# Kernel tuning notes

Measured on AMD Instinct MI355X. Metric: run time of the kernel, lower is better.

The kernel has to match this reference:

```python
import jax, jax.numpy as jnp
import numpy as np

B = 128   # batch (must equal input_size due to the transpose quirk in the source)
S = 1024  # sequence length
D = 128   # input_size
H = 256   # hidden_size


def setup_inputs() -> dict:
    key = jax.random.key(0)
    k_x, k_wf, k_wb = jax.random.split(key, 3)
    x = jax.random.normal(k_x, (B, S, D), dtype=jnp.float32)
    scale = 1.0 / np.sqrt(D + H)
    # gate order: f, i, c, o  (matches W_f, W_i, W_c, W_o in the source)
    W_fwd = jax.random.normal(k_wf, (4, H, D + H), dtype=jnp.float32) * scale
    W_bwd = jax.random.normal(k_wb, (4, H, D + H), dtype=jnp.float32) * scale
    b_fwd = jnp.zeros((4, H), dtype=jnp.float32)
    b_bwd = jnp.zeros((4, H), dtype=jnp.float32)
    return {"x": x, "W_fwd": W_fwd, "b_fwd": b_fwd, "W_bwd": W_bwd, "b_bwd": b_bwd}


def _lstm_scan(xs, W, b, h0, c0):
    """xs: (S, B, D). Faithful to source: concat is [x_t.T ; h] (needs B == D)."""
    def step(carry, xt):
        h, c = carry
        concat = jnp.concatenate([xt.T, h], axis=1)  # (B, D+H)
        z = jnp.einsum('ghk,bk->gbh', W, concat) + b[:, None, :]  # (4, B, H)
        f = jax.nn.sigmoid(z[0])
        i = jax.nn.sigmoid(z[1])
        c_tilde = jnp.tanh(z[2])
        o = jax.nn.sigmoid(z[3])
        c_next = f * c + i * c_tilde
        h_next = o * jnp.tanh(c_next)
        return (h_next, c_next), h_next
    (hT, cT), hs = jax.lax.scan(step, (h0, c0), xs)
    return hs, hT, cT


def reference(x, W_fwd, b_fwd, W_bwd, b_bwd):
    Bb, Ss, Dd = x.shape
    Hh = W_fwd.shape[1]
    h0 = jnp.zeros((Bb, Hh), dtype=x.dtype)
    c0 = jnp.zeros((Bb, Hh), dtype=x.dtype)
    xs = jnp.swapaxes(x, 0, 1)  # (S, B, D)
    # forward direction: t = 0 .. S-1
    hs_f, hT_f, cT_f = _lstm_scan(xs, W_fwd, b_fwd, h0, c0)
    # backward direction: t = S-1 .. 0
    hs_b, hT_b, cT_b = _lstm_scan(xs[::-1], W_bwd, b_bwd, h0, c0)
    out_f = jnp.swapaxes(hs_f, 0, 1)            # (B, S, H)
    out_b = jnp.swapaxes(hs_b[::-1], 0, 1)      # (B, S, H), re-reversed to time order
    output = jnp.concatenate([out_f, out_b], axis=2)  # (B, S, 2H); batch_first=False => no transpose (source quirk)
    # source mutates h0/c0 in place via views, so returned states are the FINAL states
    h_final = jnp.stack([hT_f, hT_b], axis=0)   # (2, B, H)
    c_final = jnp.stack([cT_f, cT_b], axis=0)
    return output, (h_final, c_final)
```

## Files before the change

### kernel.cpp

```cpp
#include <hip/hip_runtime.h>
#include <hip/hip_bf16.h>


typedef unsigned int  u32;
typedef unsigned long long u64;
typedef unsigned short u16;
typedef short short4_t __attribute__((ext_vector_type(4)));
typedef short short8_t __attribute__((ext_vector_type(8)));
typedef float float4_t __attribute__((ext_vector_type(4)));
typedef float float2_t __attribute__((ext_vector_type(2)));
typedef int   int4_t   __attribute__((ext_vector_type(4)));

#define S_LEN 1024
#define D_IN  128
#define H_DIM 256
#define B_DIM 128
#define K_DIM 384
#define LSTR  392
#define SMEM_BYTES ((128 + 64) * LSTR * 2)

#define WS_CNT_BYTES 65536
#define WS_HBUF  65536
#define WS_XBT   327680
#define WS_NEED  (WS_XBT + (size_t)S_LEN * B_DIM * D_IN * 2)

__device__ __forceinline__ u16 f2bf(float f) {
    union { float f; u32 u; } v; v.f = f;
    u32 r = v.u + 0x7fffu + ((v.u >> 16) & 1u);
    return (u16)(r >> 16);
}
__device__ __forceinline__ float sig_f(float x) {
    return __builtin_amdgcn_rcpf(1.f + __expf(-x));
}
__device__ __forceinline__ float tanh_f(float x) {
    return 2.f * sig_f(2.f * x) - 1.f;
}

__global__ __launch_bounds__(256, 4)
void tx_kernel(const float* __restrict__ x, u16* __restrict__ xbt)
{
    __shared__ u16 tile[128][136];
    const int t   = blockIdx.x;
    const int tid = threadIdx.x;
    for (int c = 0; c < 16; ++c) {
        int f = tid + c * 256;
        int k = f >> 5, q = f & 31;
        float4_t v = *(const float4_t*)(x + (size_t)k * (S_LEN * D_IN)
                                          + (size_t)t * D_IN + 4 * q);
        tile[4 * q + 0][k] = f2bf(v[0]);
        tile[4 * q + 1][k] = f2bf(v[1]);
        tile[4 * q + 2][k] = f2bf(v[2]);
        tile[4 * q + 3][k] = f2bf(v[3]);
    }
    __syncthreads();
    u16* dst = xbt + (size_t)t * (B_DIM * D_IN);
    for (int c = 0; c < 8; ++c) {
        int f = tid + c * 256;
        int r = f >> 4, kc = f & 15;
        *(short8_t*)(dst + r * D_IN + kc * 8) = *(const short8_t*)(&tile[r][kc * 8]);
    }
}

__global__ __launch_bounds__(256, 1)
void bilstm_kernel(const float* __restrict__ x,
                   const float* __restrict__ Wf, const float* __restrict__ bf_,
                   const float* __restrict__ Wb, const float* __restrict__ bb_,
                   float* __restrict__ out,
                   u32* __restrict__ cnt,
                   u16* __restrict__ hbuf,
                   const u16* __restrict__ xbt,
                   int use_xbt)
{
    extern __shared__ char smem[];
    u16* Wl = (u16*)smem;
    u16* Cc = (u16*)smem + 128 * LSTR;

    const int tid = threadIdx.x;
    const int bx  = blockIdx.x;
    const int dir = bx >> 4;
    const int id  = bx & 15;
    const int bg  = id >> 3;
    const int hs  = id & 7;
    const int b0  = bg * 64;
    const int h0  = hs * 32;

    const float* W    = dir ? Wb : Wf;
    const float* bias = dir ? bb_ : bf_;

    for (int it = 0; it < 48; ++it) {
        int v  = tid + it * 256;
        int r  = v / 96;
        int kv = v - r * 96;
        int g  = r >> 5, hl = r & 31;
        const float4_t src = *(const float4_t*)(W + ((g * H_DIM + h0 + hl) * K_DIM + kv * 4));
        short4_t d;
        d[0] = (short)f2bf(src[0]); d[1] = (short)f2bf(src[1]);
        d[2] = (short)f2bf(src[2]); d[3] = (short)f2bf(src[3]);
        *(short4_t*)(Wl + r * LSTR + kv * 4) = d;
    }

    const int lane = tid & 63;
    const int wid  = tid >> 6;
    const int quad = lane >> 4;
    const int l15  = lane & 15;
    const int hlt  = wid >> 1;
    const int nh   = wid & 1;

    float bias_r[4][4];
    #pragma unroll
    for (int g = 0; g < 4; ++g)
        #pragma unroll
        for (int i = 0; i < 4; ++i)
            bias_r[g][i] = bias[g * H_DIM + h0 + hlt * 16 + quad * 4 + i];

    float c_st[2][4];
    #pragma unroll
    for (int nt = 0; nt < 2; ++nt)
        #pragma unroll
        for (int i = 0; i < 4; ++i) c_st[nt][i] = 0.f;

    u32* grpcnt = cnt + (dir * 2 + bg) * (S_LEN * 4);

    __syncthreads();

    short8_t areg[4][8];
    #pragma unroll
    for (int ks = 0; ks < 8; ++ks) {
        const int ko = (ks + 4) * 32 + quad * 8;
        #pragma unroll
        for (int g = 0; g < 4; ++g)
            areg[g][ks] = *(const short8_t*)(Wl + (g * 32 + hlt * 16 + l15) * LSTR + ko);
    }

    short8_t xv[4];
    auto XLOAD = [&](int tt) {
        const u16* xs = xbt + (size_t)tt * (B_DIM * D_IN) + b0 * D_IN;
        #pragma unroll
        for (int it = 0; it < 4; ++it) {
            int f = tid + it * 256;
            int r = f >> 4, kc = f & 15;
            xv[it] = *(const short8_t*)(xs + r * D_IN + kc * 8);
        }
    };
    if (use_xbt) XLOAD(dir ? (S_LEN - 1) : 0);

    for (int s = 0; s < S_LEN; ++s) {
        const int t = dir ? (S_LEN - 1 - s) : s;

        if (use_xbt) {
            #pragma unroll
            for (int it = 0; it < 4; ++it) {
                int f = tid + it * 256;
                int r = f >> 4, kc = f & 15;
                *(short8_t*)(Cc + r * LSTR + kc * 8) = xv[it];
            }
        } else {
            const int m  = tid & 31;
            const int kb = tid >> 5;
            const float* xcol = x + (size_t)t * D_IN + b0 + 2 * m;
            for (int it = 0; it < 16; ++it) {
                int k = it * 8 + kb;
                float2_t v = *(const float2_t*)(xcol + (size_t)k * (S_LEN * D_IN));
                Cc[(2 * m) * LSTR + k]     = f2bf(v[0]);
                Cc[(2 * m + 1) * LSTR + k] = f2bf(v[1]);
            }
        }
        __syncthreads();

        float4_t acc[4][2];
        #pragma unroll
        for (int g = 0; g < 4; ++g) {
            acc[g][0] = (float4_t){0.f, 0.f, 0.f, 0.f};
            acc[g][1] = (float4_t){0.f, 0.f, 0.f, 0.f};
        }

        #pragma unroll
        for (int ks = 0; ks < 4; ++ks) {
            const int ko = ks * 32 + quad * 8;
            short8_t a[4], bb[2];
            #pragma unroll
            for (int g = 0; g < 4; ++g)
                a[g] = *(const short8_t*)(Wl + (g * 32 + hlt * 16 + l15) * LSTR + ko);
            #pragma unroll
            for (int nt = 0; nt < 2; ++nt)
                bb[nt] = *(const short8_t*)(Cc + (nh * 32 + nt * 16 + l15) * LSTR + ko);
            #pragma unroll
            for (int g = 0; g < 4; ++g)
                #pragma unroll
                for (int nt = 0; nt < 2; ++nt)
                    acc[g][nt] = __builtin_amdgcn_mfma_f32_16x16x32_bf16(
                        a[g], bb[nt], acc[g][nt], 0, 0, 0);
        }

        u16* cw = Cc + (tid >> 2) * LSTR + D_IN + 64 * (tid & 3);
        if (s > 0) {
            const u64* fp = (const u64*)(grpcnt + (s - 1) * 4);
            const u64 tgt = 0x0000000800000008ull;
            for (;;) {
                u64 w0 = __hip_atomic_load(fp,     __ATOMIC_RELAXED,
                                           __HIP_MEMORY_SCOPE_AGENT);
                u64 w1 = __hip_atomic_load(fp + 1, __ATOMIC_RELAXED,
                                           __HIP_MEMORY_SCOPE_AGENT);
                if (w0 == tgt && w1 == tgt) break;
                __builtin_amdgcn_s_sleep(1);
            }
            const int par_r = (s - 1) & 1;
            const u16* hb = hbuf + ((size_t)((dir * 2 + par_r) * B_DIM + b0 + (tid >> 2)))
                                  * H_DIM + 64 * (tid & 3);
            int4_t hv[8];
#define HL(i, OFF) asm volatile("global_load_dwordx4 %0, %1, off offset:" OFF " sc0 sc1" \
                                : "=v"(hv[i]) : "v"(hb) : "memory")
            HL(0, "0");  HL(1, "16"); HL(2, "32"); HL(3, "48");
            HL(4, "64"); HL(5, "80"); HL(6, "96"); HL(7, "112");
#undef HL
            asm volatile("s_waitcnt vmcnt(0)" ::: "memory");
            #pragma unroll
            for (int it = 0; it < 8; ++it)
                *(int4_t*)(cw + 8 * it) = hv[it];
        } else {
            int4_t z4 = (int4_t){0, 0, 0, 0};
            #pragma unroll
            for (int it = 0; it < 8; ++it)
                *(int4_t*)(cw + 8 * it) = z4;
        }
        __syncthreads();

        if (use_xbt && s + 1 < S_LEN)
            XLOAD(dir ? (S_LEN - 2 - s) : (s + 1));

        #pragma unroll
        for (int ks = 0; ks < 8; ++ks) {
            const int ko = (ks + 4) * 32 + quad * 8;
            short8_t bb0 = *(const short8_t*)(Cc + (nh * 32 + l15) * LSTR + ko);
            short8_t bb1 = *(const short8_t*)(Cc + (nh * 32 + 16 + l15) * LSTR + ko);
            #pragma unroll
            for (int g = 0; g < 4; ++g) {
                acc[g][0] = __builtin_amdgcn_mfma_f32_16x16x32_bf16(
                    areg[g][ks], bb0, acc[g][0], 0, 0, 0);
                acc[g][1] = __builtin_amdgcn_mfma_f32_16x16x32_bf16(
                    areg[g][ks], bb1, acc[g][1], 0, 0, 0);
            }
        }

        const int par_w = s & 1;
        u16* hdst = hbuf + ((dir * 2 + par_w) * B_DIM) * H_DIM;
        const int hrow = h0 + hlt * 16 + quad * 4;

        #pragma unroll
        for (int nt = 0; nt < 2; ++nt) {
            const int b = b0 + nh * 32 + nt * 16 + l15;
            float hv_[4], cv[4];
            #pragma unroll
            for (int i = 0; i < 4; ++i) {
                float zf = acc[0][nt][i] + bias_r[0][i];
                float zi = acc[1][nt][i] + bias_r[1][i];
                float zc = acc[2][nt][i] + bias_r[2][i];
                float zo = acc[3][nt][i] + bias_r[3][i];
                float fg = sig_f(zf);
                float ig = sig_f(zi);
                float og = sig_f(zo);
                float ct = tanh_f(zc);
                float c  = fg * c_st[nt][i] + ig * ct;
                c_st[nt][i] = c;
                float h  = og * tanh_f(c);
                hv_[i] = h; cv[i] = c;
            }
            u64 hp = (u64)f2bf(hv_[0]) | ((u64)f2bf(hv_[1]) << 16)
                   | ((u64)f2bf(hv_[2]) << 32) | ((u64)f2bf(hv_[3]) << 48);
            __hip_atomic_store((u64*)(hdst + b * H_DIM + hrow), hp,
                               __ATOMIC_RELAXED, __HIP_MEMORY_SCOPE_AGENT);
            float4_t ho; ho[0]=hv_[0]; ho[1]=hv_[1]; ho[2]=hv_[2]; ho[3]=hv_[3];
            *(float4_t*)(out + ((size_t)b * (S_LEN * 2 * H_DIM)
                          + (size_t)t * (2 * H_DIM) + dir * H_DIM + hrow)) = ho;
            if (s == S_LEN - 1) {
                size_t fo = (size_t)67108864 + (size_t)dir * 32768
                          + (size_t)b * H_DIM + hrow;
                *(float4_t*)(out + fo) = ho;
                float4_t co; co[0]=cv[0]; co[1]=cv[1]; co[2]=cv[2]; co[3]=cv[3];
                *(float4_t*)(out + fo + 65536) = co;
            }
        }

        asm volatile("s_waitcnt vmcnt(0)" ::: "memory");
        if (lane == 0)
            __hip_atomic_fetch_add(grpcnt + s * 4 + wid, 1u,
                                   __ATOMIC_RELAXED, __HIP_MEMORY_SCOPE_AGENT);
    }
}

extern "C" void kernel_launch(void* const* d_in, const int* in_sizes, int n_in,
                              void* d_out, int out_size, void* d_ws, size_t ws_size,
                              hipStream_t stream) {
    (void)in_sizes; (void)n_in; (void)out_size;
    hipFuncSetAttribute((const void*)bilstm_kernel,
                        hipFuncAttributeMaxDynamicSharedMemorySize, SMEM_BYTES);
    u32* cnt  = (u32*)d_ws;
    u16* hbuf = (u16*)((char*)d_ws + WS_HBUF);
    u16* xbt  = (u16*)((char*)d_ws + WS_XBT);
    const int use_xbt = (ws_size >= WS_NEED) ? 1 : 0;
    hipMemsetAsync(d_ws, 0, WS_CNT_BYTES, stream);
    if (use_xbt)
        tx_kernel<<<dim3(S_LEN), dim3(256), 0, stream>>>((const float*)d_in[0], xbt);
    bilstm_kernel<<<dim3(32), dim3(256), SMEM_BYTES, stream>>>(
        (const float*)d_in[0], (const float*)d_in[1], (const float*)d_in[2],
        (const float*)d_in[3], (const float*)d_in[4],
        (float*)d_out, cnt, hbuf, xbt, use_xbt);
}
```

Measured before the change: 5.489 ms.

## Drop shared memory staging; load MFMA fragments directly and use per-wave flags

Removes the LDS staging of weights, x and h. All weight fragments, including the x-part, stay in registers, and x and h fragments are loaded straight from global memory into MFMA operand layout. The per-step atomic counters and block-wide __syncthreads are replaced by per-wave flag slots polled wave-wide, so each wave waits only on its own dependencies. The h store and flag publish are moved ahead of the output writes to shorten the critical path. This raises register pressure (xareg plus areg plus 16 h vectors) and duplicates global loads of h across waves.

Result: slower. 6.433 ms (+17.2%).

```diff
diff --git a/kernel.cpp b/kernel.cpp
--- a/kernel.cpp
+++ b/kernel.cpp
@@ -5,10 +5,8 @@
 typedef unsigned int  u32;
 typedef unsigned long long u64;
 typedef unsigned short u16;
-typedef short short4_t __attribute__((ext_vector_type(4)));
 typedef short short8_t __attribute__((ext_vector_type(8)));
 typedef float float4_t __attribute__((ext_vector_type(4)));
-typedef float float2_t __attribute__((ext_vector_type(2)));
 typedef int   int4_t   __attribute__((ext_vector_type(4)));
 
 #define S_LEN 1024
@@ -16,12 +14,10 @@
 #define H_DIM 256
 #define B_DIM 128
 #define K_DIM 384
-#define LSTR  392
-#define SMEM_BYTES ((128 + 64) * LSTR * 2)
-
-#define WS_CNT_BYTES 65536
-#define WS_HBUF  65536
-#define WS_XBT   327680
+
+#define WS_FLAGS_BYTES 524288
+#define WS_HBUF  524288
+#define WS_XBT   786432
 #define WS_NEED  (WS_XBT + (size_t)S_LEN * B_DIM * D_IN * 2)
 
 __device__ __forceinline__ u16 f2bf(float f) {
@@ -66,15 +62,11 @@
                    const float* __restrict__ Wf, const float* __restrict__ bf_,
                    const float* __restrict__ Wb, const float* __restrict__ bb_,
                    float* __restrict__ out,
-                   u32* __restrict__ cnt,
+                   u32* __restrict__ flags,
                    u16* __restrict__ hbuf,
                    const u16* __restrict__ xbt,
                    int use_xbt)
 {
-    extern __shared__ char smem[];
-    u16* Wl = (u16*)smem;
-    u16* Cc = (u16*)smem + 128 * LSTR;
-
     const int tid = threadIdx.x;
     const int bx  = blockIdx.x;
     const int dir = bx >> 4;
@@ -83,21 +75,10 @@
     const int hs  = id & 7;
     const int b0  = bg * 64;
     const int h0  = hs * 32;
+    const int grp = dir * 2 + bg;
 
     const float* W    = dir ? Wb : Wf;
     const float* bias = dir ? bb_ : bf_;
-
-    for (int it = 0; it < 48; ++it) {
-        int v  = tid + it * 256;
-        int r  = v / 96;
-        int kv = v - r * 96;
-        int g  = r >> 5, hl = r & 31;
-        const float4_t src = *(const float4_t*)(W + ((g * H_DIM + h0 + hl) * K_DIM + kv * 4));
-        short4_t d;
-        d[0] = (short)f2bf(src[0]); d[1] = (short)f2bf(src[1]);
-        d[2] = (short)f2bf(src[2]); d[3] = (short)f2bf(src[3]);
-        *(short4_t*)(Wl + r * LSTR + kv * 4) = d;
-    }
 
     const int lane = tid & 63;
     const int wid  = tid >> 6;
@@ -106,6 +87,29 @@
     const int hlt  = wid >> 1;
     const int nh   = wid & 1;
 
+    auto WFRAG = [&](int g, int k0) -> short8_t {
+        const float* p = W + ((size_t)(g * H_DIM + h0 + hlt * 16 + l15) * K_DIM + k0);
+        float4_t v0 = *(const float4_t*)p;
+        float4_t v1 = *(const float4_t*)(p + 4);
+        short8_t d;
+        d[0] = (short)f2bf(v0[0]); d[1] = (short)f2bf(v0[1]);
+        d[2] = (short)f2bf(v0[2]); d[3] = (short)f2bf(v0[3]);
+        d[4] = (short)f2bf(v1[0]); d[5] = (short)f2bf(v1[1]);
+        d[6] = (short)f2bf(v1[2]); d[7] = (short)f2bf(v1[3]);
+        return d;
+    };
+    short8_t xareg[4][4];
+    short8_t areg[4][8];
+    #pragma unroll
+    for (int g = 0; g < 4; ++g) {
+        #pragma unroll
+        for (int ks = 0; ks < 4; ++ks)
+            xareg[g][ks] = WFRAG(g, ks * 32 + quad * 8);
+        #pragma unroll
+        for (int ks = 0; ks < 8; ++ks)
+            areg[g][ks]  = WFRAG(g, 128 + ks * 32 + quad * 8);
+    }
+
     float bias_r[4][4];
     #pragma unroll
     for (int g = 0; g < 4; ++g)
@@ -119,53 +123,62 @@
         #pragma unroll
         for (int i = 0; i < 4; ++i) c_st[nt][i] = 0.f;
 
-    u32* grpcnt = cnt + (dir * 2 + bg) * (S_LEN * 4);
-
-    __syncthreads();
-
-    short8_t areg[4][8];
-    #pragma unroll
-    for (int ks = 0; ks < 8; ++ks) {
-        const int ko = (ks + 4) * 32 + quad * 8;
-        #pragma unroll
-        for (int g = 0; g < 4; ++g)
-            areg[g][ks] = *(const short8_t*)(Wl + (g * 32 + hlt * 16 + l15) * LSTR + ko);
-    }
-
-    short8_t xv[4];
-    auto XLOAD = [&](int tt) {
-        const u16* xs = xbt + (size_t)tt * (B_DIM * D_IN) + b0 * D_IN;
-        #pragma unroll
-        for (int it = 0; it < 4; ++it) {
-            int f = tid + it * 256;
-            int r = f >> 4, kc = f & 15;
-            xv[it] = *(const short8_t*)(xs + r * D_IN + kc * 8);
+    const int myrow0 = b0 + nh * 32 + l15;
+
+    short8_t xf[8];
+    auto XFRAG = [&](int tt) {
+        if (use_xbt) {
+            const u16* xs = xbt + (size_t)tt * (B_DIM * D_IN) + quad * 8;
+            #pragma unroll
+            for (int nt = 0; nt < 2; ++nt)
+                #pragma unroll
+                for (int ks = 0; ks < 4; ++ks)
+                    xf[nt * 4 + ks] =
+                        *(const short8_t*)(xs + (myrow0 + nt * 16) * D_IN + ks * 32);
+        } else {
+            #pragma unroll
+            for (int nt = 0; nt < 2; ++nt)
+                #pragma unroll
+                for (int ks = 0; ks < 4; ++ks) {
+                    short8_t d;
+                    #pragma unroll
+                    for (int e = 0; e < 8; ++e) {
+                        int k = ks * 32 + quad * 8 + e;
+                        d[e] = (short)f2bf(x[(size_t)k * (S_LEN * D_IN)
+                                             + (size_t)tt * D_IN + myrow0 + nt * 16]);
+                    }
+                    xf[nt * 4 + ks] = d;
+                }
         }
     };
-    if (use_xbt) XLOAD(dir ? (S_LEN - 1) : 0);
+    XFRAG(dir ? (S_LEN - 1) : 0);
+
+    u32*       myflag = flags + (size_t)grp * (S_LEN * 32) + hs * 4 + wid;
+    const u32* pollw  = flags + (size_t)grp * (S_LEN * 32) + (lane & 31);
 
     for (int s = 0; s < S_LEN; ++s) {
         const int t = dir ? (S_LEN - 1 - s) : s;
 
-        if (use_xbt) {
-            #pragma unroll
-            for (int it = 0; it < 4; ++it) {
-                int f = tid + it * 256;
-                int r = f >> 4, kc = f & 15;
-                *(short8_t*)(Cc + r * LSTR + kc * 8) = xv[it];
-            }
-        } else {
-            const int m  = tid & 31;
-            const int kb = tid >> 5;
-            const float* xcol = x + (size_t)t * D_IN + b0 + 2 * m;
-            for (int it = 0; it < 16; ++it) {
-                int k = it * 8 + kb;
-                float2_t v = *(const float2_t*)(xcol + (size_t)k * (S_LEN * D_IN));
-                Cc[(2 * m) * LSTR + k]     = f2bf(v[0]);
-                Cc[(2 * m + 1) * LSTR + k] = f2bf(v[1]);
-            }
-        }
-        __syncthreads();
+        int4_t hv[16];
+        if (s > 0) {
+            const u32* fw = pollw + (size_t)(s - 1) * 32;
+            for (;;) {
+                u32 v = __hip_atomic_load(fw, __ATOMIC_RELAXED,
+                                          __HIP_MEMORY_SCOPE_AGENT);
+                if (__all((int)(v == (u32)s))) break;
+            }
+            const int par_r = (s - 1) & 1;
+            const u16* hb0 = hbuf + ((size_t)((dir * 2 + par_r) * B_DIM + myrow0))
+                                    * H_DIM + quad * 8;
+            const u16* hb1 = hb0 + 16 * H_DIM;
+#define HL(i, base, O) asm volatile("global_load_dwordx4 %0, %1, off offset:" O " sc0 sc1" \
+                                    : "=v"(hv[i]) : "v"(base) : "memory")
+            HL(0,  hb0, "0");   HL(1,  hb0, "64");  HL(2,  hb0, "128"); HL(3,  hb0, "192");
+            HL(4,  hb0, "256"); HL(5,  hb0, "320"); HL(6,  hb0, "384"); HL(7,  hb0, "448");
+            HL(8,  hb1, "0");   HL(9,  hb1, "64");  HL(10, hb1, "128"); HL(11, hb1, "192");
+            HL(12, hb1, "256"); HL(13, hb1, "320"); HL(14, hb1, "384"); HL(15, hb1, "448");
+#undef HL
+        }
 
         float4_t acc[4][2];
         #pragma unroll
@@ -173,72 +186,34 @@
             acc[g][0] = (float4_t){0.f, 0.f, 0.f, 0.f};
             acc[g][1] = (float4_t){0.f, 0.f, 0.f, 0.f};
         }
-
-        #pragma unroll
-        for (int ks = 0; ks < 4; ++ks) {
-            const int ko = ks * 32 + quad * 8;
-            short8_t a[4], bb[2];
-            #pragma unroll
-            for (int g = 0; g < 4; ++g)
-                a[g] = *(const short8_t*)(Wl + (g * 32 + hlt * 16 + l15) * LSTR + ko);
-            #pragma unroll
-            for (int nt = 0; nt < 2; ++nt)
-                bb[nt] = *(const short8_t*)(Cc + (nh * 32 + nt * 16 + l15) * LSTR + ko);
-            #pragma unroll
-            for (int g = 0; g < 4; ++g)
-                #pragma unroll
-                for (int nt = 0; nt < 2; ++nt)
-                    acc[g][nt] = __builtin_amdgcn_mfma_f32_16x16x32_bf16(
-                        a[g], bb[nt], acc[g][nt], 0, 0, 0);
-        }
-
-        u16* cw = Cc + (tid >> 2) * LSTR + D_IN + 64 * (tid & 3);
-        if (s > 0) {
-            const u64* fp = (const u64*)(grpcnt + (s - 1) * 4);
-            const u64 tgt = 0x0000000800000008ull;
-            for (;;) {
-                u64 w0 = __hip_atomic_load(fp,     __ATOMIC_RELAXED,
-                                           __HIP_MEMORY_SCOPE_AGENT);
-                u64 w1 = __hip_atomic_load(fp + 1, __ATOMIC_RELAXED,
-                                           __HIP_MEMORY_SCOPE_AGENT);
-                if (w0 == tgt && w1 == tgt) break;
-                __builtin_amdgcn_s_sleep(1);
-            }
-            const int par_r = (s - 1) & 1;
-            const u16* hb = hbuf + ((size_t)((dir * 2 + par_r) * B_DIM + b0 + (tid >> 2)))
-                                  * H_DIM + 64 * (tid & 3);
-            int4_t hv[8];
-#define HL(i, OFF) asm volatile("global_load_dwordx4 %0, %1, off offset:" OFF " sc0 sc1" \
-                                : "=v"(hv[i]) : "v"(hb) : "memory")
-            HL(0, "0");  HL(1, "16"); HL(2, "32"); HL(3, "48");
-            HL(4, "64"); HL(5, "80"); HL(6, "96"); HL(7, "112");
-#undef HL
-            asm volatile("s_waitcnt vmcnt(0)" ::: "memory");
-            #pragma unroll
-            for (int it = 0; it < 8; ++it)
-                *(int4_t*)(cw + 8 * it) = hv[it];
-        } else {
-            int4_t z4 = (int4_t){0, 0, 0, 0};
-            #pragma unroll
-            for (int it = 0; it < 8; ++it)
-                *(int4_t*)(cw + 8 * it) = z4;
-        }
-        __syncthreads();
-
-        if (use_xbt && s + 1 < S_LEN)
-            XLOAD(dir ? (S_LEN - 2 - s) : (s + 1));
-
-        #pragma unroll
-        for (int ks = 0; ks < 8; ++ks) {
-            const int ko = (ks + 4) * 32 + quad * 8;
-            short8_t bb0 = *(const short8_t*)(Cc + (nh * 32 + l15) * LSTR + ko);
-            short8_t bb1 = *(const short8_t*)(Cc + (nh * 32 + 16 + l15) * LSTR + ko);
+        #pragma unroll
+        for (int ks = 0; ks < 4; ++ks)
             #pragma unroll
             for (int g = 0; g < 4; ++g) {
                 acc[g][0] = __builtin_amdgcn_mfma_f32_16x16x32_bf16(
-                    areg[g][ks], bb0, acc[g][0], 0, 0, 0);
+                    xareg[g][ks], xf[ks],     acc[g][0], 0, 0, 0);
                 acc[g][1] = __builtin_amdgcn_mfma_f32_16x16x32_bf16(
-                    areg[g][ks], bb1, acc[g][1], 0, 0, 0);
+                    xareg[g][ks], xf[4 + ks], acc[g][1], 0, 0, 0);
+            }
+
+        const bool pf = (s + 1 < S_LEN);
+        if (pf) XFRAG(dir ? (S_LEN - 2 - s) : (s + 1));
+
+        if (s > 0) {
+            if (pf) asm volatile("s_waitcnt vmcnt(8)" ::: "memory");
+            else    asm volatile("s_waitcnt vmcnt(0)" ::: "memory");
+            __builtin_amdgcn_sched_barrier(0);
+            #pragma unroll
+            for (int ks = 0; ks < 8; ++ks) {
+                short8_t b0f = __builtin_bit_cast(short8_t, hv[ks]);
+                short8_t b1f = __builtin_bit_cast(short8_t, hv[8 + ks]);
+                #pragma unroll
+                for (int g = 0; g < 4; ++g) {
+                    acc[g][0] = __builtin_amdgcn_mfma_f32_16x16x32_bf16(
+                        areg[g][ks], b0f, acc[g][0], 0, 0, 0);
+                    acc[g][1] = __builtin_amdgcn_mfma_f32_16x16x32_bf16(
+                        areg[g][ks], b1f, acc[g][1], 0, 0, 0);
+                }
             }
         }
 
@@ -246,10 +221,9 @@
         u16* hdst = hbuf + ((dir * 2 + par_w) * B_DIM) * H_DIM;
         const int hrow = h0 + hlt * 16 + quad * 4;
 
-        #pragma unroll
-        for (int nt = 0; nt < 2; ++nt) {
-            const int b = b0 + nh * 32 + nt * 16 + l15;
-            float hv_[4], cv[4];
+        float hv_[2][4], cv_[2][4];
+        #pragma unroll
+        for (int nt = 0; nt < 2; ++nt)
             #pragma unroll
             for (int i = 0; i < 4; ++i) {
                 float zf = acc[0][nt][i] + bias_r[0][i];
@@ -262,29 +236,40 @@
                 float ct = tanh_f(zc);
                 float c  = fg * c_st[nt][i] + ig * ct;
                 c_st[nt][i] = c;
-                float h  = og * tanh_f(c);
-                hv_[i] = h; cv[i] = c;
-            }
-            u64 hp = (u64)f2bf(hv_[0]) | ((u64)f2bf(hv_[1]) << 16)
-                   | ((u64)f2bf(hv_[2]) << 32) | ((u64)f2bf(hv_[3]) << 48);
+                hv_[nt][i] = og * tanh_f(c);
+                cv_[nt][i] = c;
+            }
+
+        #pragma unroll
+        for (int nt = 0; nt < 2; ++nt) {
+            const int b = b0 + nh * 32 + nt * 16 + l15;
+            u64 hp = (u64)f2bf(hv_[nt][0]) | ((u64)f2bf(hv_[nt][1]) << 16)
+                   | ((u64)f2bf(hv_[nt][2]) << 32) | ((u64)f2bf(hv_[nt][3]) << 48);
             __hip_atomic_store((u64*)(hdst + b * H_DIM + hrow), hp,
                                __ATOMIC_RELAXED, __HIP_MEMORY_SCOPE_AGENT);
-            float4_t ho; ho[0]=hv_[0]; ho[1]=hv_[1]; ho[2]=hv_[2]; ho[3]=hv_[3];
+        }
+        asm volatile("s_waitcnt vmcnt(0)" ::: "memory");
+        if (lane == 0)
+            __hip_atomic_store(myflag + (size_t)s * 32, (u32)(s + 1),
+                               __ATOMIC_RELAXED, __HIP_MEMORY_SCOPE_AGENT);
+        __builtin_amdgcn_sched_barrier(0);
+
+        #pragma unroll
+        for (int nt = 0; nt < 2; ++nt) {
+            const int b = b0 + nh * 32 + nt * 16 + l15;
+            float4_t ho; ho[0]=hv_[nt][0]; ho[1]=hv_[nt][1];
+                         ho[2]=hv_[nt][2]; ho[3]=hv_[nt][3];
             *(float4_t*)(out + ((size_t)b * (S_LEN * 2 * H_DIM)
                           + (size_t)t * (2 * H_DIM) + dir * H_DIM + hrow)) = ho;
             if (s == S_LEN - 1) {
                 size_t fo = (size_t)67108864 + (size_t)dir * 32768
                           + (size_t)b * H_DIM + hrow;
                 *(float4_t*)(out + fo) = ho;
-                float4_t co; co[0]=cv[0]; co[1]=cv[1]; co[2]=cv[2]; co[3]=cv[3];
+                float4_t co; co[0]=cv_[nt][0]; co[1]=cv_[nt][1];
+                             co[2]=cv_[nt][2]; co[3]=cv_[nt][3];
                 *(float4_t*)(out + fo + 65536) = co;
             }
         }
-
-        asm volatile("s_waitcnt vmcnt(0)" ::: "memory");
-        if (lane == 0)
-            __hip_atomic_fetch_add(grpcnt + s * 4 + wid, 1u,
-                                   __ATOMIC_RELAXED, __HIP_MEMORY_SCOPE_AGENT);
     }
 }
 
@@ -292,17 +277,15 @@
                               void* d_out, int out_size, void* d_ws, size_t ws_size,
                               hipStream_t stream) {
     (void)in_sizes; (void)n_in; (void)out_size;
-    hipFuncSetAttribute((const void*)bilstm_kernel,
-                        hipFuncAttributeMaxDynamicSharedMemorySize, SMEM_BYTES);
-    u32* cnt  = (u32*)d_ws;
-    u16* hbuf = (u16*)((char*)d_ws + WS_HBUF);
-    u16* xbt  = (u16*)((char*)d_ws + WS_XBT);
+    u32* flags = (u32*)d_ws;
+    u16* hbuf  = (u16*)((char*)d_ws + WS_HBUF);
+    u16* xbt   = (u16*)((char*)d_ws + WS_XBT);
     const int use_xbt = (ws_size >= WS_NEED) ? 1 : 0;
-    hipMemsetAsync(d_ws, 0, WS_CNT_BYTES, stream);
+    hipMemsetAsync(d_ws, 0, WS_FLAGS_BYTES, stream);
     if (use_xbt)
         tx_kernel<<<dim3(S_LEN), dim3(256), 0, stream>>>((const float*)d_in[0], xbt);
-    bilstm_kernel<<<dim3(32), dim3(256), SMEM_BYTES, stream>>>(
+    bilstm_kernel<<<dim3(32), dim3(256), 0, stream>>>(
         (const float*)d_in[0], (const float*)d_in[1], (const float*)d_in[2],
         (const float*)d_in[3], (const float*)d_in[4],
-        (float*)d_out, cnt, hbuf, xbt, use_xbt);
-}
+        (float*)d_out, flags, hbuf, xbt, use_xbt);
+}
```
